# Performance work log

Hardware: AMD Instinct MI355X
Metric: run time of the kernel (lower is better)

## Reference

```python
import jax, jax.numpy as jnp
import numpy as np

B, F, S, H1, O = 8192, 128, 128, 64, 1

def setup_inputs() -> dict:
    key = jax.random.key(0)
    ks = jax.random.split(key, 8)
    sc1 = 1.0  # Linear(1, S): torch init ~ U(-1,1); use scaled normals
    return {
        "x":  jax.random.normal(ks[0], (B, F), dtype=jnp.float32),
        "W1": jax.random.normal(ks[1], (F, S), dtype=jnp.float32) * sc1,
        "b1": jax.random.normal(ks[2], (F, S), dtype=jnp.float32) * 0.1,
        "W2": jax.random.normal(ks[3], (F, S, H1), dtype=jnp.float32) * (1.0 / np.sqrt(S)),
        "b2": jax.random.normal(ks[4], (F, H1), dtype=jnp.float32) * 0.1,
        "W3": jax.random.normal(ks[5], (F, H1, O), dtype=jnp.float32) * (1.0 / np.sqrt(H1)),
        "b3": jax.random.normal(ks[6], (F, O), dtype=jnp.float32) * 0.1,
        "bias": jnp.zeros((O,), dtype=jnp.float32),
    }

def reference(x, W1, b1, W2, b2, W3, b3, bias):
    # Per-feature net: Linear(1,S) -> ReLU -> Linear(S,H1) -> ReLU -> (Dropout=id at eval) -> Linear(H1,O)
    # Batched over the feature axis f (equivalent to the original Python loop + cat).
    h1 = jax.nn.relu(x[:, :, None] * W1[None, :, :] + b1[None, :, :])      # [B,F,S]
    h2 = jax.nn.relu(jnp.einsum('bfs,fsh->bfh', h1, W2) + b2[None, :, :])  # [B,F,H1]
    fo = jnp.einsum('bfh,fho->bfo', h2, W3) + b3[None, :, :]               # [B,F,O]
    # torch.cat(...,dim=1) of [B,1] slices -> [B,F]; sum(dim=1,keepdim=True)+bias -> [B,1]
    out = fo.reshape(B, F * O).sum(axis=1, keepdims=True) + bias           # [B,1]
    return out
```

## Files before the change

kernel.cpp:

```cpp
#include <hip/hip_runtime.h>
#include <hip/hip_bf16.h>

#define B_ 8192
#define F_ 128
#define S_ 128
#define H_ 64

typedef __attribute__((ext_vector_type(4))) float f32x4;
typedef __attribute__((ext_vector_type(8))) short bf16x8;

__global__ __launch_bounds__(256) void nam_init(float* __restrict__ out,
                                                const float* __restrict__ bias) {
    int i = blockIdx.x * 256 + threadIdx.x;
    if (i < B_) out[i] = bias[0];
}

static __device__ __forceinline__ short f2bf(float v) {
    __hip_bfloat16 t = __float2bfloat16(v);
    return __builtin_bit_cast(short, t);
}

__global__ __launch_bounds__(256) void nam_prep(const float* __restrict__ W2,
                                                bf16x8* __restrict__ W2bf) {
    const int idx = blockIdx.x * 256 + threadIdx.x;
    const int l   = idx & 63;
    const int m   = (idx >> 6) & 3;
    const int kk  = (idx >> 8) & 3;
    const int f   = idx >> 10;
    const int l16 = l & 15, lg = l >> 4;

    const float* __restrict__ src =
        W2 + ((size_t)f * S_ + kk * 32 + lg * 8) * H_ + m * 16 + l16;
    bf16x8 v;
#pragma unroll
    for (int j = 0; j < 8; ++j) v[j] = f2bf(src[j * H_]);
    W2bf[idx] = v;
}

__global__ __launch_bounds__(256) void nam_mfma(
    const float* __restrict__ x,
    const float* __restrict__ W1,
    const float* __restrict__ b1,
    const bf16x8* __restrict__ W2bf,
    const float* __restrict__ b2,
    const float* __restrict__ W3,
    const float* __restrict__ b3,
    float* __restrict__ out)
{
    const int f   = blockIdx.x >> 5;
    const int bt  = blockIdx.x & 31;
    const int tid = threadIdx.x;
    const int w   = tid >> 6;
    const int l   = tid & 63;
    const int l16 = l & 15;
    const int lg  = l >> 4;

    const int bbase = bt * 256 + w * 64;

    const float* __restrict__ W1f = W1 + f * S_;
    const float* __restrict__ b1f = b1 + f * S_;
    const bf16x8* __restrict__ W2f = W2bf + (size_t)f * 16 * 64 + l;

    float xv[4];
#pragma unroll
    for (int n = 0; n < 4; ++n)
        xv[n] = x[(size_t)(bbase + n * 16 + l16) * F_ + f];

    f32x4 acc[4][4];
#pragma unroll
    for (int m = 0; m < 4; ++m)
#pragma unroll
        for (int n = 0; n < 4; ++n)
            acc[m][n] = (f32x4){0.f, 0.f, 0.f, 0.f};

#pragma unroll
    for (int kk = 0; kk < 4; ++kk) {
        const int s0 = kk * 32 + lg * 8;

        bf16x8 afrag[4];
#pragma unroll
        for (int m = 0; m < 4; ++m)
            afrag[m] = W2f[(kk * 4 + m) * 64];

        const f32x4 w1a = *(const f32x4*)(W1f + s0);
        const f32x4 w1b = *(const f32x4*)(W1f + s0 + 4);
        const f32x4 b1a = *(const f32x4*)(b1f + s0);
        const f32x4 b1b = *(const f32x4*)(b1f + s0 + 4);

        bf16x8 bfrag[4];
#pragma unroll
        for (int n = 0; n < 4; ++n) {
#pragma unroll
            for (int j = 0; j < 4; ++j) {
                bfrag[n][j]     = f2bf(fmaxf(fmaf(xv[n], w1a[j], b1a[j]), 0.f));
                bfrag[n][j + 4] = f2bf(fmaxf(fmaf(xv[n], w1b[j], b1b[j]), 0.f));
            }
        }

#pragma unroll
        for (int m = 0; m < 4; ++m)
#pragma unroll
            for (int n = 0; n < 4; ++n)
                acc[m][n] = __builtin_amdgcn_mfma_f32_16x16x32_bf16(
                    afrag[m], bfrag[n], acc[m][n], 0, 0, 0);
    }

    const float* __restrict__ b2f = b2 + f * H_;
    const float* __restrict__ W3f = W3 + f * H_;
    f32x4 b2v[4], w3v[4];
#pragma unroll
    for (int m = 0; m < 4; ++m) {
        b2v[m] = *(const f32x4*)(b2f + m * 16 + lg * 4);
        w3v[m] = *(const f32x4*)(W3f + m * 16 + lg * 4);
    }
    const float b3f = b3[f];

#pragma unroll
    for (int n = 0; n < 4; ++n) {
        float fo = 0.f;
#pragma unroll
        for (int m = 0; m < 4; ++m)
#pragma unroll
            for (int r = 0; r < 4; ++r)
                fo = fmaf(fmaxf(acc[m][n][r] + b2v[m][r], 0.f), w3v[m][r], fo);
        fo += __shfl_xor(fo, 16);
        fo += __shfl_xor(fo, 32);
        if (lg == 0)
            atomicAdd(&out[bbase + n * 16 + l16], fo + b3f);
    }
}

extern "C" void kernel_launch(void* const* d_in, const int* in_sizes, int n_in,
                              void* d_out, int out_size, void* d_ws, size_t ws_size,
                              hipStream_t stream) {
    const float* x    = (const float*)d_in[0];
    const float* W1   = (const float*)d_in[1];
    const float* b1   = (const float*)d_in[2];
    const float* W2   = (const float*)d_in[3];
    const float* b2   = (const float*)d_in[4];
    const float* W3   = (const float*)d_in[5];
    const float* b3   = (const float*)d_in[6];
    const float* bias = (const float*)d_in[7];
    float* out = (float*)d_out;
    bf16x8* W2bf = (bf16x8*)d_ws;

    nam_init<<<(B_ + 255) / 256, 256, 0, stream>>>(out, bias);
    nam_prep<<<(F_ * 16 * 64) / 256, 256, 0, stream>>>(W2, W2bf);
    nam_mfma<<<F_ * (B_ / 256), 256, 0, stream>>>(x, W1, b1, W2bf, b2, W3, b3, out);
}
```

Before: 110.4 us.

## Halve per-wave batch tile, transpose x for coalesced loads, raise occupancy

Each wave now covers 32 batch rows instead of 64, halving the accumulator registers, and the block count doubles. Launch bounds now request 4 blocks per CU and the k-loop is no longer unrolled, which should allow more waves in flight. A new transpose kernel writes x as feature-major into workspace so the per-feature x loads are contiguous, falling back to strided loads if the workspace is too small. The cost is an extra kernel launch plus a full pass over x, twice as many atomics on the output, and twice as many redundant W2 fragment loads across blocks.

```diff
diff --git a/kernel.cpp b/kernel.cpp
--- a/kernel.cpp
+++ b/kernel.cpp
@@ -37,8 +37,25 @@
     W2bf[idx] = v;
 }
 
-__global__ __launch_bounds__(256) void nam_mfma(
+__global__ __launch_bounds__(256) void nam_xt(const float* __restrict__ x,
+                                              float* __restrict__ xT) {
+    __shared__ float t[32][33];
+    const int li = threadIdx.x & 31;
+    const int wi = threadIdx.x >> 5;
+    const int b0 = (blockIdx.x & 255) * 32;
+    const int f0 = (blockIdx.x >> 8) * 32;
+#pragma unroll
+    for (int r = wi; r < 32; r += 8)
+        t[r][li] = x[(size_t)(b0 + r) * F_ + f0 + li];
+    __syncthreads();
+#pragma unroll
+    for (int r = wi; r < 32; r += 8)
+        xT[(size_t)(f0 + r) * B_ + b0 + li] = t[li][r];
+}
+
+__global__ __launch_bounds__(256, 4) void nam_mfma(
     const float* __restrict__ x,
+    const float* __restrict__ xT,
     const float* __restrict__ W1,
     const float* __restrict__ b1,
     const bf16x8* __restrict__ W2bf,
@@ -47,86 +64,87 @@
     const float* __restrict__ b3,
     float* __restrict__ out)
 {
-    const int f   = blockIdx.x >> 5;
-    const int bt  = blockIdx.x & 31;
+    const int f   = blockIdx.x >> 6;
+    const int bt  = blockIdx.x & 63;
     const int tid = threadIdx.x;
     const int w   = tid >> 6;
     const int l   = tid & 63;
     const int l16 = l & 15;
     const int lg  = l >> 4;
 
-    const int bbase = bt * 256 + w * 64;
+    const int bbase = bt * 128 + w * 32;
 
     const float* __restrict__ W1f = W1 + f * S_;
     const float* __restrict__ b1f = b1 + f * S_;
     const bf16x8* __restrict__ W2f = W2bf + (size_t)f * 16 * 64 + l;
 
-    float xv[4];
+    float xv0, xv1;
+    if (xT) {
+        xv0 = xT[(size_t)f * B_ + bbase + l16];
+        xv1 = xT[(size_t)f * B_ + bbase + 16 + l16];
+    } else {
+        xv0 = x[(size_t)(bbase + l16) * F_ + f];
+        xv1 = x[(size_t)(bbase + 16 + l16) * F_ + f];
+    }
+
+    f32x4 acc[4][2];
 #pragma unroll
-    for (int n = 0; n < 4; ++n)
-        xv[n] = x[(size_t)(bbase + n * 16 + l16) * F_ + f];
+    for (int m = 0; m < 4; ++m) {
+        acc[m][0] = (f32x4){0.f, 0.f, 0.f, 0.f};
+        acc[m][1] = (f32x4){0.f, 0.f, 0.f, 0.f};
+    }
 
-    f32x4 acc[4][4];
-#pragma unroll
-    for (int m = 0; m < 4; ++m)
-#pragma unroll
-        for (int n = 0; n < 4; ++n)
-            acc[m][n] = (f32x4){0.f, 0.f, 0.f, 0.f};
-
-#pragma unroll
+#pragma unroll 1
     for (int kk = 0; kk < 4; ++kk) {
-        const int s0 = kk * 32 + lg * 8;
-
         bf16x8 afrag[4];
 #pragma unroll
         for (int m = 0; m < 4; ++m)
             afrag[m] = W2f[(kk * 4 + m) * 64];
 
+        const int s0 = kk * 32 + lg * 8;
         const f32x4 w1a = *(const f32x4*)(W1f + s0);
         const f32x4 w1b = *(const f32x4*)(W1f + s0 + 4);
         const f32x4 b1a = *(const f32x4*)(b1f + s0);
         const f32x4 b1b = *(const f32x4*)(b1f + s0 + 4);
 
-        bf16x8 bfrag[4];
+        bf16x8 bf0, bf1;
 #pragma unroll
-        for (int n = 0; n < 4; ++n) {
-#pragma unroll
-            for (int j = 0; j < 4; ++j) {
-                bfrag[n][j]     = f2bf(fmaxf(fmaf(xv[n], w1a[j], b1a[j]), 0.f));
-                bfrag[n][j + 4] = f2bf(fmaxf(fmaf(xv[n], w1b[j], b1b[j]), 0.f));
-            }
+        for (int j = 0; j < 4; ++j) {
+            bf0[j]     = f2bf(fmaxf(fmaf(xv0, w1a[j], b1a[j]), 0.f));
+            bf0[j + 4] = f2bf(fmaxf(fmaf(xv0, w1b[j], b1b[j]), 0.f));
+            bf1[j]     = f2bf(fmaxf(fmaf(xv1, w1a[j], b1a[j]), 0.f));
+            bf1[j + 4] = f2bf(fmaxf(fmaf(xv1, w1b[j], b1b[j]), 0.f));
         }
 
 #pragma unroll
-        for (int m = 0; m < 4; ++m)
-#pragma unroll
-            for (int n = 0; n < 4; ++n)
-                acc[m][n] = __builtin_amdgcn_mfma_f32_16x16x32_bf16(
-                    afrag[m], bfrag[n], acc[m][n], 0, 0, 0);
+        for (int m = 0; m < 4; ++m) {
+            acc[m][0] = __builtin_amdgcn_mfma_f32_16x16x32_bf16(afrag[m], bf0, acc[m][0], 0, 0, 0);
+            acc[m][1] = __builtin_amdgcn_mfma_f32_16x16x32_bf16(afrag[m], bf1, acc[m][1], 0, 0, 0);
+        }
     }
 
     const float* __restrict__ b2f = b2 + f * H_;
     const float* __restrict__ W3f = W3 + f * H_;
-    f32x4 b2v[4], w3v[4];
+    const float b3f = b3[f];
+
+    float fo0 = 0.f, fo1 = 0.f;
 #pragma unroll
     for (int m = 0; m < 4; ++m) {
-        b2v[m] = *(const f32x4*)(b2f + m * 16 + lg * 4);
-        w3v[m] = *(const f32x4*)(W3f + m * 16 + lg * 4);
+        const f32x4 b2v = *(const f32x4*)(b2f + m * 16 + lg * 4);
+        const f32x4 w3v = *(const f32x4*)(W3f + m * 16 + lg * 4);
+#pragma unroll
+        for (int r = 0; r < 4; ++r) {
+            fo0 = fmaf(fmaxf(acc[m][0][r] + b2v[r], 0.f), w3v[r], fo0);
+            fo1 = fmaf(fmaxf(acc[m][1][r] + b2v[r], 0.f), w3v[r], fo1);
+        }
     }
-    const float b3f = b3[f];
-
-#pragma unroll
-    for (int n = 0; n < 4; ++n) {
-        float fo = 0.f;
-#pragma unroll
-        for (int m = 0; m < 4; ++m)
-#pragma unroll
-            for (int r = 0; r < 4; ++r)
-                fo = fmaf(fmaxf(acc[m][n][r] + b2v[m][r], 0.f), w3v[m][r], fo);
-        fo += __shfl_xor(fo, 16);
-        fo += __shfl_xor(fo, 32);
-        if (lg == 0)
-            atomicAdd(&out[bbase + n * 16 + l16], fo + b3f);
+    fo0 += __shfl_xor(fo0, 16);
+    fo0 += __shfl_xor(fo0, 32);
+    fo1 += __shfl_xor(fo1, 16);
+    fo1 += __shfl_xor(fo1, 32);
+    if (lg == 0) {
+        atomicAdd(&out[bbase + l16], fo0 + b3f);
+        atomicAdd(&out[bbase + 16 + l16], fo1 + b3f);
     }
 }
 
@@ -142,9 +160,16 @@
     const float* b3   = (const float*)d_in[6];
     const float* bias = (const float*)d_in[7];
     float* out = (float*)d_out;
+
     bf16x8* W2bf = (bf16x8*)d_ws;
+    const size_t W2BF_BYTES = (size_t)F_ * 16 * 64 * 16;
+    const size_t XT_BYTES   = (size_t)F_ * B_ * 4;
+    float* xT = (ws_size >= W2BF_BYTES + XT_BYTES)
+                    ? (float*)((char*)d_ws + W2BF_BYTES) : nullptr;
 
     nam_init<<<(B_ + 255) / 256, 256, 0, stream>>>(out, bias);
     nam_prep<<<(F_ * 16 * 64) / 256, 256, 0, stream>>>(W2, W2bf);
-    nam_mfma<<<F_ * (B_ / 256), 256, 0, stream>>>(x, W1, b1, W2bf, b2, W3, b3, out);
+    if (xT)
+        nam_xt<<<(B_ / 32) * (F_ / 32), 256, 0, stream>>>(x, xT);
+    nam_mfma<<<F_ * (B_ / 128), 256, 0, stream>>>(x, xT, W1, b1, W2bf, b2, W3, b3, out);
 }
```

After: 119.6 us. 1.08x slower.
